# Kernel tuning notes

Hardware: AMD Instinct MI355X
Metric: run time of the kernel (lower is better)

The kernel has to match this reference:

```python
import jax, jax.numpy as jnp
import numpy as np

KEEP_ID, DEL_ID, PAD_ID, STOP_ID, ANNO_ID = 1, 2, 0, 102, 103
V, E, H = 21128, 768, 768
B, T = 8, 256
S = T + 1  # org/simp length; S = T+1 guarantees counters never go out of range


def setup_inputs() -> dict:
    key = jax.random.key(0)
    ks = jax.random.split(key, 16)
    def p(i, shape, scale):
        return jax.random.normal(ks[i], shape, jnp.float32) * scale
    return {
        "input_edits": jax.random.randint(ks[0], (B, T), 0, V),
        "org_ids": jax.random.randint(ks[1], (B, S), 0, V),
        "simp_sent": jax.random.randint(ks[2], (B, S), 0, V),
        "h0": jax.random.normal(ks[3], (B, H), jnp.float32),
        "c0": jax.random.normal(ks[4], (B, H), jnp.float32),
        "encoder_outputs_org": jax.random.normal(ks[5], (B, S, E), jnp.float32),
        "emb": p(6, (V, E), 0.02),
        "Wih_e": p(7, (4 * H, E), 0.03), "Whh_e": p(8, (4 * H, H), 0.03), "b_e": jnp.zeros((4 * H,), jnp.float32),
        "Wih_w": p(9, (4 * H, E), 0.03), "Whh_w": p(10, (4 * H, H), 0.03), "b_w": jnp.zeros((4 * H,), jnp.float32),
        "W_attn": p(11, (H, H), 0.03),
        "W_align": p(12, (H, E), 0.03),
        "W_mlp": p(13, (E, 4 * H), 0.03), "b_mlp": jnp.zeros((E,), jnp.float32),
        "W_out": p(14, (V, E), 0.02), "b_out": jnp.zeros((V,), jnp.float32),
    }


def lstm(x, h0, c0, Wih, Whh, b):
    # x: [B,T,E]; single-layer batch_first LSTM, torch gate order (i,f,g,o)
    def step(carry, xt):
        h, c = carry
        g = xt @ Wih.T + h @ Whh.T + b
        i, f, gg, o = jnp.split(g, 4, axis=-1)
        c2 = jax.nn.sigmoid(f) * c + jax.nn.sigmoid(i) * jnp.tanh(gg)
        h2 = jax.nn.sigmoid(o) * jnp.tanh(c2)
        return (h2, c2), h2
    (hT, cT), hs = jax.lax.scan(step, (h0, c0), jnp.swapaxes(x, 0, 1))
    return jnp.swapaxes(hs, 0, 1), hT, cT


def reference(input_edits, org_ids, simp_sent, h0, c0, encoder_outputs_org,
              emb, Wih_e, Whh_e, b_e, Wih_w, Whh_w, b_w,
              W_attn, W_align, W_mlp, b_mlp, W_out, b_out):
    bsz, nsteps = input_edits.shape
    enc = jnp.tanh(encoder_outputs_org @ W_align.T)            # [B,S,H]
    out_edits, hT, cT = lstm(emb[input_edits], h0, c0, Wih_e, Whh_e, b_e)  # [B,T,H]
    out_words, _, _ = lstm(emb[simp_sent], h0, c0, Wih_w, Whh_w, b_w)      # [B,S,H]

    key = out_edits @ W_attn.T                                  # [B,T,H]
    attn = jax.nn.softmax(jnp.einsum('bth,bsh->bts', key, enc), axis=-1)
    ctx = jnp.einsum('bts,bsh->bth', attn, enc)                 # [B,T,H]

    # counter recurrence (pre-update counters are used for the gathers at step t)
    gold = jnp.swapaxes(input_edits[:, 1:], 0, 1)               # [T-1, B]
    bidx = jnp.arange(bsz)

    def cstep(carry, a):
        kd, ki, an = carry
        kd2 = kd + ((a == KEEP_ID) | (a == DEL_ID)).astype(kd.dtype)
        not_special = (a != DEL_ID) & (a != STOP_ID) & (a != PAD_ID)
        ki2 = ki + not_special.astype(ki.dtype)
        is_ins = not_special & (a != KEEP_ID)
        next_is_anno = org_ids[bidx, an + 1] == ANNO_ID
        an2 = jnp.where(is_ins & next_is_anno, an + 1, jnp.maximum(kd2, an))
        return (kd2, ki2, an2), (ki, an)

    z = jnp.zeros((bsz,), jnp.int32)
    _, (ki_seq, an_seq) = jax.lax.scan(cstep, (z, z, z), gold)
    ki_bt = jnp.swapaxes(ki_seq, 0, 1)                          # [B,T-1]
    an_bt = jnp.swapaxes(an_seq, 0, 1)                          # [B,T-1]

    c = jnp.take_along_axis(enc, an_bt[:, :, None], axis=1)        # [B,T-1,H]
    c_word = jnp.take_along_axis(out_words, ki_bt[:, :, None], axis=1)  # [B,T-1,H]

    Tm1 = nsteps - 1
    feat = jnp.concatenate([out_edits[:, :Tm1], ctx[:, :Tm1], c, c_word], axis=-1)  # [B,T-1,4H]
    mlp = jnp.tanh(feat @ W_mlp.T + b_mlp)                      # [B,T-1,E]
    logp = jax.nn.log_softmax(mlp @ W_out.T + b_out, axis=-1)   # [B,T-1,V]
    return logp, hT, cT
```

## Files before the change

### kernel.cpp

```cpp
#include <hip/hip_runtime.h>
#include <hip/hip_bf16.h>

typedef short s16x8 __attribute__((ext_vector_type(8)));
typedef float f32x4 __attribute__((ext_vector_type(4)));
typedef unsigned short u16;
typedef unsigned short u16x4 __attribute__((ext_vector_type(4)));
typedef unsigned long long u64;
typedef unsigned long long u64x2 __attribute__((ext_vector_type(2)));

__device__ __forceinline__ u16 f2bf(float f) {
  __hip_bfloat16 h = __float2bfloat16(f);
  u16 u;
  __builtin_memcpy(&u, &h, sizeof(u));
  return u;
}
__device__ __forceinline__ float bf2f(u16 u) {
  unsigned int x = ((unsigned int)u) << 16;
  float f;
  __builtin_memcpy(&f, &x, 4);
  return f;
}

__device__ __forceinline__ unsigned int a_ld32(const unsigned int* p) {
  return __hip_atomic_load(p, __ATOMIC_RELAXED, __HIP_MEMORY_SCOPE_AGENT);
}
__device__ __forceinline__ u64 a_ld64(const u64* p) {
  return __hip_atomic_load(p, __ATOMIC_RELAXED, __HIP_MEMORY_SCOPE_AGENT);
}
__device__ __forceinline__ void a_st32(unsigned int* p, unsigned int v) {
  __hip_atomic_store(p, v, __ATOMIC_RELAXED, __HIP_MEMORY_SCOPE_AGENT);
}

__device__ __forceinline__ void gload16(const void* g, void* l) {
  __builtin_amdgcn_global_load_lds(
      (const __attribute__((address_space(1))) unsigned int*)g,
      (__attribute__((address_space(3))) unsigned int*)l, 16, 0, 0);
}

template<int CBF16, int GATHER, int TANHA, int BIAS, int SWAPXY>
__global__ __launch_bounds__(256) void gemm_bt(
    const u16* __restrict__ A, const u16* __restrict__ B,
    const float* __restrict__ bias, void* __restrict__ Cv,
    const int* __restrict__ ids,
    int M, int N, int K, int lda, int ldb, int ldc,
    long sAz, long sBz, long sCz, int rpb, long cbs,
    const int* __restrict__ ids2, const float* __restrict__ bias2, int dM)
{
  __shared__ u16 sA[4096];
  __shared__ u16 sB[4096];
  const int tid = threadIdx.x;
  const int z = blockIdx.z;
  if (z) {
    if (dM) M += dM;
    if (ids2) ids = ids2;
    if (bias2) bias = bias2;
  }
  const int m0 = (SWAPXY ? blockIdx.x : blockIdx.y) * 128;
  const int n0 = (SWAPXY ? blockIdx.y : blockIdx.x) * 128;
  const u16* Ab = A + z * sAz;
  const u16* Bb = B + z * sBz;
  const int w = tid >> 6, lane = tid & 63;
  const int wr = w >> 1, wc = w & 1;
  const int lr = lane & 15, lk = lane >> 4;
  f32x4 acc[4][4] = {};
  const int e0 = tid * 8, e1 = e0 + 2048;
  const int r0 = e0 >> 5, c0 = e0 & 31;
  const int r1 = e1 >> 5, c1 = e1 & 31;
  long arow0, arow1;
  if (GATHER) {
    int i0 = m0 + r0; if (i0 >= M) i0 = M - 1;
    int i1 = m0 + r1; if (i1 >= M) i1 = M - 1;
    arow0 = (long)ids[i0] * lda;
    arow1 = (long)ids[i1] * lda;
  } else {
    arow0 = (long)(m0 + r0) * lda;
    arow1 = (long)(m0 + r1) * lda;
  }
  const long brow0 = (long)(n0 + r0) * ldb;
  const long brow1 = (long)(n0 + r1) * ldb;
  char* sAc = (char*)sA;
  char* sBc = (char*)sB;
  const size_t cb = (size_t)w * 1024;
  for (int kt = 0; kt < K; kt += 32) {
    __syncthreads();
    gload16(Ab + arow0 + kt + c0, sAc + cb);
    gload16(Ab + arow1 + kt + c1, sAc + 4096 + cb);
    gload16(Bb + brow0 + kt + c0, sBc + cb);
    gload16(Bb + brow1 + kt + c1, sBc + 4096 + cb);
    __syncthreads();
    s16x8 af[4], bf[4];
#pragma unroll
    for (int i = 0; i < 4; i++) {
      af[i] = *(const s16x8*)&sA[(wr*64 + i*16 + lr)*32 + lk*8];
      bf[i] = *(const s16x8*)&sB[(wc*64 + i*16 + lr)*32 + lk*8];
    }
#pragma unroll
    for (int mi = 0; mi < 4; mi++)
#pragma unroll
      for (int ni = 0; ni < 4; ni++)
        acc[mi][ni] = __builtin_amdgcn_mfma_f32_16x16x32_bf16(af[mi], bf[ni], acc[mi][ni], 0, 0, 0);
  }
#pragma unroll
  for (int mi = 0; mi < 4; mi++) {
#pragma unroll
    for (int ni = 0; ni < 4; ni++) {
#pragma unroll
      for (int r = 0; r < 4; r++) {
        int gm = m0 + wr*64 + mi*16 + lk*4 + r;
        int gn = n0 + wc*64 + ni*16 + lr;
        if (gm < M && gn < N) {
          float v = acc[mi][ni][r];
          if (BIAS) v += bias[gn];
          if (TANHA) v = tanhf(v);
          long ci = z * sCz + (long)(gm / rpb) * cbs + (long)(gm % rpb) * ldc + gn;
          if (CBF16) ((u16*)Cv)[ci] = f2bf(v);
          else       ((float*)Cv)[ci] = v;
        }
      }
    }
  }
}

__global__ __launch_bounds__(256) void gemm_mlp(
    const u16* __restrict__ oute, const u16* __restrict__ ctxp,
    const u16* __restrict__ encp, const u16* __restrict__ outw,
    const int* __restrict__ ki_bt, const int* __restrict__ an_bt,
    const u16* __restrict__ B, const float* __restrict__ bias,
    u16* __restrict__ C)
{
  __shared__ u16 sA[4096];
  __shared__ u16 sB[4096];
  const int tid = threadIdx.x;
  const int m0 = blockIdx.y * 128, n0 = blockIdx.x * 128;
  const int w = tid >> 6, lane = tid & 63;
  const int wr = w >> 1, wc = w & 1;
  const int lr = lane & 15, lk = lane >> 4;
  f32x4 acc[4][4] = {};
  const int e0 = tid * 8, e1 = e0 + 2048;
  const int r0 = e0 >> 5, c0 = e0 & 31;
  const int r1 = e1 >> 5, c1 = e1 & 31;
  const u16 *b00, *b01, *b02, *b03, *b10, *b11, *b12, *b13;
  {
    int m = m0 + r0; if (m >= 2040) m = 2039;
    int b = m / 255, t = m - b * 255;
    b00 = oute + ((long)(b * 256 + t)) * 768;
    b01 = ctxp + ((long)(b * 256 + t)) * 768;
    b02 = encp + ((long)(b * 384 + an_bt[m])) * 768;
    b03 = outw + ((long)(b * 256 + ki_bt[m])) * 768;
    m = m0 + r1; if (m >= 2040) m = 2039;
    b = m / 255; t = m - b * 255;
    b10 = oute + ((long)(b * 256 + t)) * 768;
    b11 = ctxp + ((long)(b * 256 + t)) * 768;
    b12 = encp + ((long)(b * 384 + an_bt[m])) * 768;
    b13 = outw + ((long)(b * 256 + ki_bt[m])) * 768;
  }
  const long brow0 = (long)(n0 + r0) * 3072;
  const long brow1 = (long)(n0 + r1) * 3072;
  char* sAc = (char*)sA;
  char* sBc = (char*)sB;
  const size_t cb = (size_t)w * 1024;
  for (int kt = 0; kt < 3072; kt += 32) {
    const int seg = kt / 768, off = kt - seg * 768;
    const u16* a0 = (seg == 0 ? b00 : seg == 1 ? b01 : seg == 2 ? b02 : b03) + off + c0;
    const u16* a1 = (seg == 0 ? b10 : seg == 1 ? b11 : seg == 2 ? b12 : b13) + off + c1;
    __syncthreads();
    gload16(a0, sAc + cb);
    gload16(a1, sAc + 4096 + cb);
    gload16(B + brow0 + kt + c0, sBc + cb);
    gload16(B + brow1 + kt + c1, sBc + 4096 + cb);
    __syncthreads();
    s16x8 af[4], bf[4];
#pragma unroll
    for (int i = 0; i < 4; i++) {
      af[i] = *(const s16x8*)&sA[(wr*64 + i*16 + lr)*32 + lk*8];
      bf[i] = *(const s16x8*)&sB[(wc*64 + i*16 + lr)*32 + lk*8];
    }
#pragma unroll
    for (int mi = 0; mi < 4; mi++)
#pragma unroll
      for (int ni = 0; ni < 4; ni++)
        acc[mi][ni] = __builtin_amdgcn_mfma_f32_16x16x32_bf16(af[mi], bf[ni], acc[mi][ni], 0, 0, 0);
  }
#pragma unroll
  for (int mi = 0; mi < 4; mi++) {
#pragma unroll
    for (int ni = 0; ni < 4; ni++) {
#pragma unroll
      for (int r = 0; r < 4; r++) {
        int gm = m0 + wr*64 + mi*16 + lk*4 + r;
        int gn = n0 + wc*64 + ni*16 + lr;
        if (gm < 2040 && gn < 768) {
          float v = tanhf(acc[mi][ni][r] + bias[gn]);
          C[(long)gm * 768 + gn] = f2bf(v);
        }
      }
    }
  }
}

__global__ __launch_bounds__(256) void cast_pre(
    const float* __restrict__ emb,
    const float* __restrict__ Wihe, u16* __restrict__ Wihe_bf,
    const float* __restrict__ Wihw, u16* __restrict__ Wihw_bf,
    const float* __restrict__ Walign, u16* __restrict__ Walign_bf,
    const float* __restrict__ encoder, u16* __restrict__ encd_bf,
    u16* __restrict__ gath_bf,
    const int* __restrict__ input_edits, const int* __restrict__ simp_sent,
    const int* __restrict__ org_ids,
    int* __restrict__ ki_bt, int* __restrict__ an_bt,
    unsigned int* __restrict__ tags)
{
  int r = blockIdx.x;
  if (r == 13312) {
    int b = threadIdx.x;
    tags[b] = 0;
    if (b >= 8) return;
    int kd = 0, ki = 0, an = 0;
    for (int t = 0; t < 255; t++) {
      int a = input_edits[b * 256 + t + 1];
      ki_bt[b * 255 + t] = ki;
      an_bt[b * 255 + t] = an;
      int kd2 = kd + ((a == 1) || (a == 2) ? 1 : 0);
      int ns = (a != 2) && (a != 102) && (a != 0);
      int ki2 = ki + (ns ? 1 : 0);
      int is_ins = ns && (a != 1);
      int nia = (org_ids[b * 257 + an + 1] == 103);
      int mx = (kd2 > an) ? kd2 : an;
      int an2 = (is_ins && nia) ? (an + 1) : mx;
      kd = kd2; ki = ki2; an = an2;
    }
    return;
  }
  const float* src; u16* dst; int valid, cols;
  if (r < 3072)                   { src=Wihe + (long)r*768;   dst=Wihe_bf + (long)r*768;   valid=1; cols=768; }
  else if ((r -= 3072) < 3072)    { src=Wihw + (long)r*768;   dst=Wihw_bf + (long)r*768;   valid=1; cols=768; }
  else if ((r -= 3072) < 768)     { src=Walign + (long)r*768; dst=Walign_bf + (long)r*768; valid=1; cols=768; }
  else if ((r -= 768) < 2176)     { src=encoder + (long)r*768; dst=encd_bf + (long)r*768;  valid=(r<2056); cols=768; }
  else if ((r -= 2176) < 2048)    { src=emb + (long)input_edits[r]*768; dst=gath_bf + (long)r*768; valid=1; cols=768; }
  else { r -= 2048;                 int ok=(r<2056);
                                    src=emb + (ok ? (long)simp_sent[r]*768 : 0); 
                                    dst=gath_bf + (long)(2048+r)*768; valid=ok; cols=768; }
  for (int c = threadIdx.x; c < cols; c += 256) {
    float v = valid ? src[c] : 0.f;
    dst[c] = f2bf(v);
  }
}

__global__ __launch_bounds__(256, 1) void lstm_persist(
    const float* __restrict__ Whh_e, const float* __restrict__ Whh_w,
    const float* __restrict__ xW_e, const float* __restrict__ xW_w,
    const float* __restrict__ h0, const float* __restrict__ c0,
    u16* __restrict__ hglob, unsigned int* __restrict__ tags,
    u16* __restrict__ out_e, u16* __restrict__ out_w,
    float* __restrict__ out_tail,
    const float* __restrict__ Wout, u16* __restrict__ Wout_bf,
    const float* __restrict__ Wmlp, u16* __restrict__ Wmlp_bf,
    const float* __restrict__ Wattn, u16* __restrict__ Wattn_bf,
    const u16* __restrict__ enc_bf, u16* __restrict__ encT_bf)
{
  const int wg = blockIdx.x;
  const int tid = threadIdx.x;

  __shared__ u16 ldsh[12288];
  __shared__ float Gbuf[16][4][2][16];

  if (wg >= 48) {
    const int swg = wg - 48;
    u16 (*tile)[33] = (u16(*)[33])ldsh;
    const int TOT = 21248 + 768 + 768 + 1728;
    for (int u = swg; u < TOT; u += 208) {
      if (u < 21248) {
        const float* src = Wout + (long)u * 768;
        u16* dst = Wout_bf + (long)u * 768;
        bool ok = (u < 21128);
        for (int c = tid; c < 768; c += 256)
          dst[c] = f2bf(ok ? src[c] : 0.f);
      } else if (u < 22016) {
        int r = u - 21248;
        const float* src = Wmlp + (long)r * 3072;
        u16* dst = Wmlp_bf + (long)r * 3072;
        for (int c = tid; c < 3072; c += 256)
          dst[c] = f2bf(src[c]);
      } else if (u < 22784) {
        int r = u - 22016;
        const float* src = Wattn + (long)r * 768;
        u16* dst = Wattn_bf + (long)r * 768;
        for (int c = tid; c < 768; c += 256)
          dst[c] = f2bf(src[c]);
      } else {
        int tau = u - 22784;
        int s0 = (tau % 9) * 32;
        int rem = tau / 9;
        int hh0 = (rem % 24) * 32;
        int b = rem / 24;
        const int tx = tid & 31, ty = tid >> 5;
#pragma unroll
        for (int i = 0; i < 32; i += 8) {
          int s = s0 + ty + i;
          u16 v = (s < 257) ? enc_bf[((long)b * 384 + s) * 768 + hh0 + tx] : (u16)0;
          tile[ty + i][tx] = v;
        }
        __syncthreads();
#pragma unroll
        for (int i = 0; i < 32; i += 8) {
          int h = hh0 + ty + i;
          encT_bf[((long)b * 768 + h) * 288 + s0 + tx] = tile[tx][ty + i];
        }
        __syncthreads();
      }
    }
    return;
  }

  const int l = wg / 24, grp = wg % 24;
  const int u0 = grp * 32;
  const int w = tid >> 6, lane = tid & 63;
  const int c16 = lane & 15, half = lane >> 4;
  const int uh = w >> 1, g0 = (w & 1) * 2;

  s16x8 wfrag[2][24];
  {
    const float* Wbase = l ? Whh_w : Whh_e;
#pragma unroll
    for (int g = 0; g < 2; g++) {
      const float* Wsrc = Wbase + (long)((g0 + g) * 768 + u0 + uh * 16 + c16) * 768 + half * 8;
#pragma unroll
      for (int s = 0; s < 24; s++) {
        float4 f0 = *(const float4*)(Wsrc + s * 32);
        float4 f1 = *(const float4*)(Wsrc + s * 32 + 4);
        s16x8 v;
        v[0]=f2bf(f0.x); v[1]=f2bf(f0.y); v[2]=f2bf(f0.z); v[3]=f2bf(f0.w);
        v[4]=f2bf(f1.x); v[5]=f2bf(f1.y); v[6]=f2bf(f1.z); v[7]=f2bf(f1.w);
        wfrag[g][s] = v;
      }
    }
  }

  const int ub = tid >> 4, j2 = (tid & 15) * 2;
  const int uA = u0 + j2;
  float creg0 = 0.f, creg1 = 0.f;
  if (tid < 128) {
    creg0 = c0[ub * 768 + uA];
    creg1 = c0[ub * 768 + uA + 1];
  }

  u16* hg = hglob + l * 24576;
  unsigned int* tg = tags + l * 64;
  const int swA = uA ^ ((ub & 7) << 3);

  if (tid < 128) {
    float v0 = h0[ub * 768 + uA], v1 = h0[ub * 768 + uA + 1];
    u16 h0a = f2bf(v0), h0b = f2bf(v1);
    u16 l0a = f2bf(v0 - bf2f(h0a)), l0b = f2bf(v1 - bf2f(h0b));
    a_st32((unsigned int*)&hg[ub * 768 + swA],
           (unsigned int)h0a | ((unsigned int)h0b << 16));
    a_st32((unsigned int*)&hg[(ub + 8) * 768 + swA],
           (unsigned int)l0a | ((unsigned int)l0b << 16));
  }
  __syncthreads();
  if (tid == 0) a_st32(&tg[grp], 1u);

  const int trow = l ? 257 : 256;
  const float* xrb = (l ? xW_w : xW_e) + ((long)ub * trow) * 3072 + uA;
  u16* outp = (l ? out_w : out_e) + (long)ub * 256 * 768 + uA;
  float2 xq0, xq1, xq2, xq3;
  if (tid < 128) {
    xq0 = *(const float2*)&xrb[0];
    xq1 = *(const float2*)&xrb[768];
    xq2 = *(const float2*)&xrb[1536];
    xq3 = *(const float2*)&xrb[2304];
  }

  for (int t = 0; t < 256; t++) {
    float2 nx0, nx1, nx2, nx3;
    if (tid < 128) {
      const float* xn = xrb + (long)(t + 1) * 3072;
      nx0 = *(const float2*)&xn[0];
      nx1 = *(const float2*)&xn[768];
      nx2 = *(const float2*)&xn[1536];
      nx3 = *(const float2*)&xn[2304];
    }

    {
      const unsigned int tgt = (unsigned int)(t + 1);
      const unsigned int* tp = tg + (t & 1) * 32;
      const bool need = (lane < 24) && (lane != grp);
      while (true) {
        unsigned int v = need ? a_ld32(&tp[lane]) : tgt;
        if (!__any(v < tgt)) break;
        __builtin_amdgcn_s_sleep(1);
      }
      asm volatile("" ::: "memory");
    }

    {
      const u64* hs8 = (const u64*)(hg + (t & 1) * 12288);
#pragma unroll
      for (int i = 0; i < 6; i++) {
        const int idx = i * 256 + tid;
        u64 a = a_ld64(&hs8[idx * 2 + 0]);
        u64 b = a_ld64(&hs8[idx * 2 + 1]);
        u64x2 vv; vv[0] = a; vv[1] = b;
        *(u64x2*)&ldsh[idx * 8] = vv;
      }
    }
    __syncthreads();

    f32x4 acc0 = {}, acc1 = {};
#pragma unroll
    for (int s = 0; s < 24; s++) {
      const int off = (c16 * 768 + s * 32 + half * 8) ^ ((c16 & 7) << 3);
      s16x8 a = *(const s16x8*)&ldsh[off];
      acc0 = __builtin_amdgcn_mfma_f32_16x16x32_bf16(a, wfrag[0][s], acc0, 0, 0, 0);
      acc1 = __builtin_amdgcn_mfma_f32_16x16x32_bf16(a, wfrag[1][s], acc1, 0, 0, 0);
    }
#pragma unroll
    for (int r = 0; r < 4; r++) {
      Gbuf[half * 4 + r][g0 + 0][uh][c16] = acc0[r];
      Gbuf[half * 4 + r][g0 + 1][uh][c16] = acc1[r];
    }
    __syncthreads();

    unsigned int hip = 0;
    float h20 = 0.f, h21 = 0.f, c20 = 0.f, c21 = 0.f;
    if (tid < 128) {
      const int uh0 = j2 >> 4, uc0 = j2 & 15;
      const int uc1 = (j2 + 1) & 15;
      float gi0 = Gbuf[ub][0][uh0][uc0] + Gbuf[ub + 8][0][uh0][uc0] + xq0.x;
      float gf0 = Gbuf[ub][1][uh0][uc0] + Gbuf[ub + 8][1][uh0][uc0] + xq1.x;
      float gg0 = Gbuf[ub][2][uh0][uc0] + Gbuf[ub + 8][2][uh0][uc0] + xq2.x;
      float go0 = Gbuf[ub][3][uh0][uc0] + Gbuf[ub + 8][3][uh0][uc0] + xq3.x;
      float gi1 = Gbuf[ub][0][uh0][uc1] + Gbuf[ub + 8][0][uh0][uc1] + xq0.y;
      float gf1 = Gbuf[ub][1][uh0][uc1] + Gbuf[ub + 8][1][uh0][uc1] + xq1.y;
      float gg1 = Gbuf[ub][2][uh0][uc1] + Gbuf[ub + 8][2][uh0][uc1] + xq2.y;
      float go1 = Gbuf[ub][3][uh0][uc1] + Gbuf[ub + 8][3][uh0][uc1] + xq3.y;
      float si0 = 1.f / (1.f + expf(-gi0)), si1 = 1.f / (1.f + expf(-gi1));
      float sf0 = 1.f / (1.f + expf(-gf0)), sf1 = 1.f / (1.f + expf(-gf1));
      float so0 = 1.f / (1.f + expf(-go0)), so1 = 1.f / (1.f + expf(-go1));
      c20 = sf0 * creg0 + si0 * tanhf(gg0);
      c21 = sf1 * creg1 + si1 * tanhf(gg1);
      h20 = so0 * tanhf(c20);
      h21 = so1 * tanhf(c21);
      creg0 = c20; creg1 = c21;
      u16 hiA = f2bf(h20), hiB = f2bf(h21);
      u16 loA = f2bf(h20 - bf2f(hiA)), loB = f2bf(h21 - bf2f(hiB));
      hip = (unsigned int)hiA | ((unsigned int)hiB << 16);
      unsigned int lop = (unsigned int)loA | ((unsigned int)loB << 16);
      u16* hb = hg + ((t + 1) & 1) * 12288;
      a_st32((unsigned int*)&hb[ub * 768 + swA], hip);
      a_st32((unsigned int*)&hb[(ub + 8) * 768 + swA], lop);
      xq0 = nx0; xq1 = nx1; xq2 = nx2; xq3 = nx3;
    }
    __syncthreads();
    if (tid == 0)
      a_st32(&tg[((t + 1) & 1) * 32 + grp], (unsigned int)(t + 2));

    if (tid < 128) {
      *(unsigned int*)&outp[(long)t * 768] = hip;
      if (l == 0 && t == 255) {
        *(float2*)&out_tail[43101120 + ub * 768 + uA] = make_float2(h20, h21);
        *(float2*)&out_tail[43107264 + ub * 768 + uA] = make_float2(c20, c21);
      }
    }
  }
}

__global__ __launch_bounds__(256) void softmax_k(
    const float* __restrict__ scores, u16* __restrict__ attn)
{
  const int row = blockIdx.x;
  const float* src = scores + (long)row * 288;
  u16* dst = attn + (long)row * 288;
  const int tid = threadIdx.x;
  float v0 = (tid < 257) ? src[tid] : -1e30f;
  float v1 = (tid + 256 < 257) ? src[tid + 256] : -1e30f;
  float mx = fmaxf(v0, v1);
  for (int o = 32; o; o >>= 1) mx = fmaxf(mx, __shfl_xor(mx, o));
  __shared__ float sm[4];
  __shared__ float ss[4];
  if ((tid & 63) == 0) sm[tid >> 6] = mx;
  __syncthreads();
  mx = fmaxf(fmaxf(sm[0], sm[1]), fmaxf(sm[2], sm[3]));
  float e0 = (tid < 257) ? expf(v0 - mx) : 0.f;
  float e1 = (tid + 256 < 257) ? expf(v1 - mx) : 0.f;
  float s = e0 + e1;
  for (int o = 32; o; o >>= 1) s += __shfl_xor(s, o);
  if ((tid & 63) == 0) ss[tid >> 6] = s;
  __syncthreads();
  s = ss[0] + ss[1] + ss[2] + ss[3];
  float inv = 1.f / s;
  dst[tid] = f2bf(e0 * inv);
  if (tid + 256 < 288) dst[tid + 256] = f2bf(e1 * inv);
}

__global__ __launch_bounds__(256) void logsoftmax_k(float* __restrict__ logits)
{
  const int m = blockIdx.x;
  float* row = logits + (long)m * 21128;
  const int tid = threadIdx.x;
  float mx = -1e30f, sm = 0.f;
  for (int i = tid * 4; i < 21128; i += 1024) {
    float4 v = *(const float4*)(row + i);
    float m4 = fmaxf(fmaxf(v.x, v.y), fmaxf(v.z, v.w));
    if (m4 > mx) { sm *= expf(mx - m4); mx = m4; }
    sm += expf(v.x - mx) + expf(v.y - mx) + expf(v.z - mx) + expf(v.w - mx);
  }
  for (int o = 32; o; o >>= 1) {
    float mo = __shfl_xor(mx, o), so = __shfl_xor(sm, o);
    float nm = fmaxf(mx, mo);
    sm = sm * expf(mx - nm) + so * expf(mo - nm);
    mx = nm;
  }
  __shared__ float wm[4], wsum[4];
  __shared__ float srs;
  if ((tid & 63) == 0) { wm[tid >> 6] = mx; wsum[tid >> 6] = sm; }
  __syncthreads();
  if (tid == 0) {
    float M = wm[0], S = wsum[0];
    for (int i = 1; i < 4; i++) {
      float nm = fmaxf(M, wm[i]);
      S = S * expf(M - nm) + wsum[i] * expf(wm[i] - nm);
      M = nm;
    }
    srs = M + logf(S);
  }
  __syncthreads();
  const float rs = srs;
  for (int i = tid * 4; i < 21128; i += 1024) {
    float4 v = *(const float4*)(row + i);
    v.x -= rs; v.y -= rs; v.z -= rs; v.w -= rs;
    *(float4*)(row + i) = v;
  }
}

extern "C" void kernel_launch(void* const* d_in, const int* in_sizes, int n_in,
                              void* d_out, int out_size, void* d_ws, size_t ws_size,
                              hipStream_t stream) {
  (void)in_sizes; (void)n_in; (void)out_size; (void)ws_size;
  const int*   input_edits = (const int*)d_in[0];
  const int*   org_ids     = (const int*)d_in[1];
  const int*   simp_sent   = (const int*)d_in[2];
  const float* h0      = (const float*)d_in[3];
  const float* c0      = (const float*)d_in[4];
  const float* encoder = (const float*)d_in[5];
  const float* emb     = (const float*)d_in[6];
  const float* Wih_e   = (const float*)d_in[7];
  const float* Whh_e   = (const float*)d_in[8];
  const float* b_e     = (const float*)d_in[9];
  const float* Wih_w   = (const float*)d_in[10];
  const float* Whh_w   = (const float*)d_in[11];
  const float* b_w     = (const float*)d_in[12];
  const float* W_attn  = (const float*)d_in[13];
  const float* W_align = (const float*)d_in[14];
  const float* W_mlp   = (const float*)d_in[15];
  const float* b_mlp   = (const float*)d_in[16];
  const float* W_out   = (const float*)d_in[17];
  const float* b_out   = (const float*)d_in[18];

  float* out = (float*)d_out;
  float* xW_e = out;
  float* xW_w = out + 2048L * 3072;
  u16* encd_bf = (u16*)(out + 2048L * 3072 + 2056L * 3072);

  char* p = (char*)d_ws;
  auto alloc = [&](size_t bytes) -> char* {
    char* r = p; p += (bytes + 255) & ~(size_t)255; return r;
  };
  u16* Wout_bf   = (u16*)alloc(21248L * 768 * 2);
  u16* Wihe_bf   = (u16*)alloc(3072L * 768 * 2);
  u16* Wihw_bf   = (u16*)alloc(3072L * 768 * 2);
  u16* Wmlp_bf   = (u16*)alloc(768L * 3072 * 2);
  u16* Walign_bf = (u16*)alloc(768L * 768 * 2);
  u16* Wattn_bf  = (u16*)alloc(768L * 768 * 2);
  u16* gath_bf   = (u16*)alloc(4224L * 768 * 2);
  u16* enc_bf    = (u16*)alloc(8L * 384 * 768 * 2);
  u16* encT_bf   = (u16*)alloc(8L * 768 * 288 * 2);
  u16* oute_bf   = (u16*)alloc(2048L * 768 * 2);
  u16* outw_bf   = (u16*)alloc(2048L * 768 * 2);
  u16* key_bf    = (u16*)alloc(2048L * 768 * 2);
  u16* attn_bf   = (u16*)alloc(8L * 256 * 288 * 2);
  u16* ctx_bf    = (u16*)alloc(2048L * 768 * 2);
  u16* mlp_bf    = (u16*)alloc(2048L * 768 * 2);
  float* scores  = (float*)alloc(8L * 256 * 288 * 4);
  u16* hglob     = (u16*)alloc(2L * 2 * 12288 * 2);
  unsigned int* tags = (unsigned int*)alloc(256 * 4);
  int* ki_bt     = (int*)alloc(2048 * 4);
  int* an_bt     = (int*)alloc(2048 * 4);

  dim3 blk(256);
  const int BIGR = 1 << 30;

  cast_pre<<<13313, blk, 0, stream>>>(emb, Wih_e, Wihe_bf, Wih_w, Wihw_bf,
                                      W_align, Walign_bf, encoder, encd_bf,
                                      gath_bf, input_edits, simp_sent,
                                      org_ids, ki_bt, an_bt, tags);

  gemm_bt<1, 0, 1, 0, 0><<<dim3(6, 17, 1), blk, 0, stream>>>(
      encd_bf, Walign_bf, nullptr, enc_bf, nullptr,
      2056, 768, 768, 768, 768, 768, 0, 0, 0, 257, 294912L,
      nullptr, nullptr, 0);

  gemm_bt<0, 0, 0, 1, 0><<<dim3(24, 17, 2), blk, 0, stream>>>(
      gath_bf, Wihe_bf, b_e, xW_e, nullptr,
      2048, 3072, 768, 768, 768, 3072, 1572864L, 2359296L, 6291456L, BIGR, 0,
      nullptr, b_w, 8);

  lstm_persist<<<256, blk, 0, stream>>>(
      Whh_e, Whh_w, xW_e, xW_w, h0, c0, hglob, tags,
      oute_bf, outw_bf, out,
      W_out, Wout_bf, W_mlp, Wmlp_bf, W_attn, Wattn_bf, enc_bf, encT_bf);

  gemm_bt<1, 0, 0, 0, 0><<<dim3(6, 16, 1), blk, 0, stream>>>(
      oute_bf, Wattn_bf, nullptr, key_bf, nullptr,
      2048, 768, 768, 768, 768, 768, 0, 0, 0, BIGR, 0,
      nullptr, nullptr, 0);
  gemm_bt<0, 0, 0, 0, 0><<<dim3(3, 2, 8), blk, 0, stream>>>(
      key_bf, enc_bf, nullptr, scores, nullptr,
      256, 257, 768, 768, 768, 288, 196608L, 294912L, 73728L, BIGR, 0,
      nullptr, nullptr, 0);
  softmax_k<<<2048, blk, 0, stream>>>(scores, attn_bf);
  gemm_bt<1, 0, 0, 0, 0><<<dim3(6, 2, 8), blk, 0, stream>>>(
      attn_bf, encT_bf, nullptr, ctx_bf, nullptr,
      256, 768, 288, 288, 288, 768, 73728L, 221184L, 196608L, BIGR, 0,
      nullptr, nullptr, 0);

  gemm_mlp<<<dim3(6, 16), blk, 0, stream>>>(
      oute_bf, ctx_bf, enc_bf, outw_bf, ki_bt, an_bt,
      Wmlp_bf, b_mlp, mlp_bf);

  gemm_bt<0, 0, 0, 1, 1><<<dim3(16, 166, 1), blk, 0, stream>>>(
      mlp_bf, Wout_bf, b_out, out, nullptr,
      2040, 21128, 768, 768, 768, 21128, 0, 0, 0, BIGR, 0,
      nullptr, nullptr, 0);

  logsoftmax_k<<<2040, blk, 0, stream>>>(out);
}
```

Before: 1.646 ms.

## Fuse per-tile softmax max/sum statistics into output GEMM epilogue

After: 1.714 ms. 4.1% more time.

```diff
diff --git a/kernel.cpp b/kernel.cpp
--- a/kernel.cpp
+++ b/kernel.cpp
@@ -37,17 +37,19 @@
       (__attribute__((address_space(3))) unsigned int*)l, 16, 0, 0);
 }
 
-template<int CBF16, int GATHER, int TANHA, int BIAS, int SWAPXY>
+template<int CBF16, int GATHER, int TANHA, int BIAS, int SWAPXY, int STATS>
 __global__ __launch_bounds__(256) void gemm_bt(
     const u16* __restrict__ A, const u16* __restrict__ B,
     const float* __restrict__ bias, void* __restrict__ Cv,
     const int* __restrict__ ids,
     int M, int N, int K, int lda, int ldb, int ldc,
     long sAz, long sBz, long sCz, int rpb, long cbs,
-    const int* __restrict__ ids2, const float* __restrict__ bias2, int dM)
+    const int* __restrict__ ids2, const float* __restrict__ bias2, int dM,
+    float* __restrict__ pmax, float* __restrict__ psum)
 {
   __shared__ u16 sA[4096];
   __shared__ u16 sB[4096];
+  __shared__ float sstat[128][2][2];
   const int tid = threadIdx.x;
   const int z = blockIdx.z;
   if (z) {
@@ -57,6 +59,8 @@
   }
   const int m0 = (SWAPXY ? blockIdx.x : blockIdx.y) * 128;
   const int n0 = (SWAPXY ? blockIdx.y : blockIdx.x) * 128;
+  const int nt = (SWAPXY ? blockIdx.y : blockIdx.x);
+  const int gridN = (SWAPXY ? gridDim.y : gridDim.x);
   const u16* Ab = A + z * sAz;
   const u16* Bb = B + z * sBz;
   const int w = tid >> 6, lane = tid & 63;
@@ -116,6 +120,57 @@
           if (CBF16) ((u16*)Cv)[ci] = f2bf(v);
           else       ((float*)Cv)[ci] = v;
         }
+      }
+    }
+  }
+  if (STATS) {
+#pragma unroll
+    for (int mi = 0; mi < 4; mi++) {
+#pragma unroll
+      for (int r = 0; r < 4; r++) {
+        float m = -1e30f, s = 0.f;
+#pragma unroll
+        for (int ni = 0; ni < 4; ni++) {
+          int gn = n0 + wc*64 + ni*16 + lr;
+          if (gn < N) {
+            float v = acc[mi][ni][r];
+            if (BIAS) v += bias[gn];
+            m = fmaxf(m, v);
+          }
+        }
+#pragma unroll
+        for (int ni = 0; ni < 4; ni++) {
+          int gn = n0 + wc*64 + ni*16 + lr;
+          if (gn < N) {
+            float v = acc[mi][ni][r];
+            if (BIAS) v += bias[gn];
+            s += expf(v - m);
+          }
+        }
+#pragma unroll
+        for (int off = 1; off < 16; off <<= 1) {
+          float mo = __shfl_xor(m, off), so = __shfl_xor(s, off);
+          float nm = fmaxf(m, mo);
+          s = s * expf(m - nm) + so * expf(mo - nm);
+          m = nm;
+        }
+        if (lr == 0) {
+          int row = wr*64 + mi*16 + lk*4 + r;
+          sstat[row][wc][0] = m;
+          sstat[row][wc][1] = s;
+        }
+      }
+    }
+    __syncthreads();
+    if (tid < 128) {
+      int gm = m0 + tid;
+      if (gm < M) {
+        float ma = sstat[tid][0][0], sa = sstat[tid][0][1];
+        float mb = sstat[tid][1][0], sb = sstat[tid][1][1];
+        float nm = fmaxf(ma, mb);
+        float s = sa * expf(ma - nm) + sb * expf(mb - nm);
+        pmax[(long)gm * gridN + nt] = nm;
+        psum[(long)gm * gridN + nt] = s;
       }
     }
   }
@@ -493,27 +548,27 @@
   if (tid + 256 < 288) dst[tid + 256] = f2bf(e1 * inv);
 }
 
-__global__ __launch_bounds__(256) void logsoftmax_k(float* __restrict__ logits)
+__global__ __launch_bounds__(256) void logsoftmax_k(
+    float* __restrict__ logits,
+    const float* __restrict__ pmax, const float* __restrict__ psum)
 {
   const int m = blockIdx.x;
-  float* row = logits + (long)m * 21128;
   const int tid = threadIdx.x;
-  float mx = -1e30f, sm = 0.f;
-  for (int i = tid * 4; i < 21128; i += 1024) {
-    float4 v = *(const float4*)(row + i);
-    float m4 = fmaxf(fmaxf(v.x, v.y), fmaxf(v.z, v.w));
-    if (m4 > mx) { sm *= expf(mx - m4); mx = m4; }
-    sm += expf(v.x - mx) + expf(v.y - mx) + expf(v.z - mx) + expf(v.w - mx);
-  }
-  for (int o = 32; o; o >>= 1) {
-    float mo = __shfl_xor(mx, o), so = __shfl_xor(sm, o);
-    float nm = fmaxf(mx, mo);
-    sm = sm * expf(mx - nm) + so * expf(mo - nm);
-    mx = nm;
+  float mm = -1e30f, ss = 0.f;
+  if (tid < 166) {
+    mm = pmax[(long)m * 166 + tid];
+    ss = psum[(long)m * 166 + tid];
+  }
+#pragma unroll
+  for (int off = 1; off < 64; off <<= 1) {
+    float mo = __shfl_xor(mm, off), so = __shfl_xor(ss, off);
+    float nm = fmaxf(mm, mo);
+    ss = ss * expf(mm - nm) + so * expf(mo - nm);
+    mm = nm;
   }
   __shared__ float wm[4], wsum[4];
   __shared__ float srs;
-  if ((tid & 63) == 0) { wm[tid >> 6] = mx; wsum[tid >> 6] = sm; }
+  if ((tid & 63) == 0) { wm[tid >> 6] = mm; wsum[tid >> 6] = ss; }
   __syncthreads();
   if (tid == 0) {
     float M = wm[0], S = wsum[0];
@@ -526,6 +581,7 @@
   }
   __syncthreads();
   const float rs = srs;
+  float* row = logits + (long)m * 21128;
   for (int i = tid * 4; i < 21128; i += 1024) {
     float4 v = *(const float4*)(row + i);
     v.x -= rs; v.y -= rs; v.z -= rs; v.w -= rs;
@@ -586,6 +642,8 @@
   unsigned int* tags = (unsigned int*)alloc(256 * 4);
   int* ki_bt     = (int*)alloc(2048 * 4);
   int* an_bt     = (int*)alloc(2048 * 4);
+  float* pmax    = (float*)alloc(2040L * 166 * 4);
+  float* psum    = (float*)alloc(2040L * 166 * 4);
 
   dim3 blk(256);
   const int BIGR = 1 << 30;
@@ -595,43 +653,43 @@
                                       gath_bf, input_edits, simp_sent,
                                       org_ids, ki_bt, an_bt, tags);
 
-  gemm_bt<1, 0, 1, 0, 0><<<dim3(6, 17, 1), blk, 0, stream>>>(
+  gemm_bt<1, 0, 1, 0, 0, 0><<<dim3(6, 17, 1), blk, 0, stream>>>(
       encd_bf, Walign_bf, nullptr, enc_bf, nullptr,
       2056, 768, 768, 768, 768, 768, 0, 0, 0, 257, 294912L,
-      nullptr, nullptr, 0);
-
-  gemm_bt<0, 0, 0, 1, 0><<<dim3(24, 17, 2), blk, 0, stream>>>(
+      nullptr, nullptr, 0, nullptr, nullptr);
+
+  gemm_bt<0, 0, 0, 1, 0, 0><<<dim3(24, 17, 2), blk, 0, stream>>>(
       gath_bf, Wihe_bf, b_e, xW_e, nullptr,
       2048, 3072, 768, 768, 768, 3072, 1572864L, 2359296L, 6291456L, BIGR, 0,
-      nullptr, b_w, 8);
+      nullptr, b_w, 8, nullptr, nullptr);
 
   lstm_persist<<<256, blk, 0, stream>>>(
       Whh_e, Whh_w, xW_e, xW_w, h0, c0, hglob, tags,
       oute_bf, outw_bf, out,
       W_out, Wout_bf, W_mlp, Wmlp_bf, W_attn, Wattn_bf, enc_bf, encT_bf);
 
-  gemm_bt<1, 0, 0, 0, 0><<<dim3(6, 16, 1), blk, 0, stream>>>(
+  gemm_bt<1, 0, 0, 0, 0, 0><<<dim3(6, 16, 1), blk, 0, stream>>>(
       oute_bf, Wattn_bf, nullptr, key_bf, nullptr,
       2048, 768, 768, 768, 768, 768, 0, 0, 0, BIGR, 0,
-      nullptr, nullptr, 0);
-  gemm_bt<0, 0, 0, 0, 0><<<dim3(3, 2, 8), blk, 0, stream>>>(
+      nullptr, nullptr, 0, nullptr, nullptr);
+  gemm_bt<0, 0, 0, 0, 0, 0><<<dim3(3, 2, 8), blk, 0, stream>>>(
       key_bf, enc_bf, nullptr, scores, nullptr,
       256, 257, 768, 768, 768, 288, 196608L, 294912L, 73728L, BIGR, 0,
-      nullptr, nullptr, 0);
+      nullptr, nullptr, 0, nullptr, nullptr);
   softmax_k<<<2048, blk, 0, stream>>>(scores, attn_bf);
-  gemm_bt<1, 0, 0, 0, 0><<<dim3(6, 2, 8), blk, 0, stream>>>(
+  gemm_bt<1, 0, 0, 0, 0, 0><<<dim3(6, 2, 8), blk, 0, stream>>>(
       attn_bf, encT_bf, nullptr, ctx_bf, nullptr,
       256, 768, 288, 288, 288, 768, 73728L, 221184L, 196608L, BIGR, 0,
-      nullptr, nullptr, 0);
+      nullptr, nullptr, 0, nullptr, nullptr);
 
   gemm_mlp<<<dim3(6, 16), blk, 0, stream>>>(
       oute_bf, ctx_bf, enc_bf, outw_bf, ki_bt, an_bt,
       Wmlp_bf, b_mlp, mlp_bf);
 
-  gemm_bt<0, 0, 0, 1, 1><<<dim3(16, 166, 1), blk, 0, stream>>>(
+  gemm_bt<0, 0, 0, 1, 1, 1><<<dim3(16, 166, 1), blk, 0, stream>>>(
       mlp_bf, Wout_bf, b_out, out, nullptr,
       2040, 21128, 768, 768, 768, 21128, 0, 0, 0, BIGR, 0,
-      nullptr, nullptr, 0);
-
-  logsoftmax_k<<<2040, blk, 0, stream>>>(out);
-}
+      nullptr, nullptr, 0, pmax, psum);
+
+  logsoftmax_k<<<2040, blk, 0, stream>>>(out, pmax, psum);
+}
```
